# Performance work log

Hardware: AMD Instinct MI355X
Metric: run time of the kernel (lower is better)

The kernel has to match this reference:

```python
import jax, jax.numpy as jnp
import numpy as np

EMBED = 768
HEADS = 12
HEAD = EMBED // HEADS  # 64
NO_ROPE = 1
GRID = 32
S_IMG = GRID * GRID
SEQ = S_IMG + NO_ROPE
BATCH = 8
SCALE = HEAD ** -0.5


def _rope_tables():
    # VisionRotaryEmbeddingFast(dim=half_head_dim=HEAD//2, pt_seq_len=GRID)
    dim = HEAD // 2  # 32 per spatial axis
    inv_freq = 1.0 / (10000.0 ** (np.arange(0, dim, 2, dtype=np.float32) / dim))  # [dim//2]
    t = np.arange(GRID, dtype=np.float32)
    f = t[:, None] * inv_freq[None, :]              # [GRID, dim//2]
    f = np.repeat(f, 2, axis=-1)                    # interleaved pairs -> [GRID, dim]
    fh = np.broadcast_to(f[:, None, :], (GRID, GRID, dim))
    fw = np.broadcast_to(f[None, :, :], (GRID, GRID, dim))
    freqs = np.concatenate([fh, fw], axis=-1).reshape(S_IMG, HEAD)  # [S_IMG, HEAD]
    return jnp.asarray(np.cos(freqs)), jnp.asarray(np.sin(freqs))

ROPE_COS, ROPE_SIN = _rope_tables()


def _rel_pos_index():
    ch, cw = np.meshgrid(np.arange(GRID), np.arange(GRID), indexing='ij')
    coords = np.stack([ch.ravel(), cw.ravel()])          # [2, S_IMG]
    rel = coords[:, :, None] - coords[:, None, :]        # [2, S_IMG, S_IMG]
    rel = rel.transpose(1, 2, 0).astype(np.int64)
    rel[:, :, 0] += GRID - 1
    rel[:, :, 1] += GRID - 1
    rel[:, :, 0] *= 2 * GRID - 1
    return jnp.asarray(rel.sum(-1))                      # [S_IMG, S_IMG]

REL_INDEX = _rel_pos_index()


def _rotate_half(x):
    # pairs are interleaved: (d r) with r=2
    x2 = x.reshape(*x.shape[:-1], -1, 2)
    return jnp.stack([-x2[..., 1], x2[..., 0]], axis=-1).reshape(x.shape)


def _apply_rope(t):
    # t: [B, H, S, HEAD]; first NO_ROPE tokens bypass rope
    t_cls, t_img = t[:, :, :NO_ROPE, :], t[:, :, NO_ROPE:, :]
    t_img = t_img * ROPE_COS + _rotate_half(t_img) * ROPE_SIN
    return jnp.concatenate([t_cls, t_img], axis=2)


def setup_inputs() -> dict:
    key = jax.random.key(0)
    ks = jax.random.split(key, 6)
    std = EMBED ** -0.5
    return {
        'x': jax.random.normal(ks[0], (BATCH, SEQ, EMBED), jnp.float32),
        'qkv_w': jax.random.normal(ks[1], (3 * EMBED, EMBED), jnp.float32) * std,
        'qkv_b': jnp.zeros((3 * EMBED,), jnp.float32),
        'proj_w': jax.random.normal(ks[2], (EMBED, EMBED), jnp.float32) * std,
        'proj_b': jnp.zeros((EMBED,), jnp.float32),
        'rel_bias_table': jax.random.normal(ks[3], ((2 * GRID - 1) * (2 * GRID - 1), HEADS), jnp.float32) * 0.02,
        'key_padding_mask': jnp.zeros((BATCH, SEQ), jnp.bool_),
    }


def reference(x, qkv_w, qkv_b, proj_w, proj_b, rel_bias_table, key_padding_mask):
    B, S, _ = x.shape
    qkv = x @ qkv_w.T + qkv_b                                  # [B,S,3E]
    qkv = qkv.reshape(B, S, 3, HEADS, HEAD).transpose(2, 0, 3, 1, 4)
    q, k, v = qkv[0], qkv[1], qkv[2]                            # [B,H,S,D]
    q = _apply_rope(q)
    k = _apply_rope(k)
    scores = jnp.einsum('bhqd,bhkd->bhqk', q, k) * SCALE        # [B,H,S,S]
    # relative position bias on image-token sub-block
    bias = rel_bias_table[REL_INDEX]                            # [S_IMG,S_IMG,H]
    bias = bias.transpose(2, 0, 1)                              # [H,S_IMG,S_IMG]
    scores = scores.at[:, :, NO_ROPE:, NO_ROPE:].add(bias[None])
    neg = jnp.finfo(scores.dtype).min
    scores = jnp.where(key_padding_mask[:, None, None, :], neg, scores)
    attn = jax.nn.softmax(scores, axis=-1)
    ctx = jnp.einsum('bhqk,bhkd->bhqd', attn, v)
    ctx = ctx.transpose(0, 2, 1, 3).reshape(B, S, EMBED)
    return ctx @ proj_w.T + proj_b
```

## Files before the change

### kernel.cpp

```cpp
#include <hip/hip_runtime.h>
#include <math.h>

#define EMBED 768
#define NHEADS 12
#define HDIM 64
#define SEQ 1025
#define NBATCH 8
#define BHCOUNT (NBATCH*NHEADS)
#define MROWS (NBATCH*SEQ)
#define QKV_N (3*EMBED)
#define QKV_ELEMS (BHCOUNT*SEQ*HDIM)
#define BT_N 3969
#define MASKPAD 1088
#define QMUL 0.1803368801111204f
#define LOG2E 1.4426950408889634f
#define NX4 1574400
#define NW4 442368
#define NP4 147456

typedef __attribute__((ext_vector_type(8))) short bf16x8;
typedef __attribute__((ext_vector_type(4))) float f32x4;
typedef __attribute__((ext_vector_type(16))) float f32x16;
typedef __attribute__((ext_vector_type(4))) unsigned int u32x4;

#define FM3(a,b,c) fmaxf(fmaxf((a),(b)),(c))

static __device__ inline unsigned short f2bf(float f) {
    unsigned u = __float_as_uint(f);
    unsigned r = (u + 0x7FFF + ((u >> 16) & 1)) >> 16;
    return (unsigned short)r;
}

static __device__ inline unsigned int cvtpk(float a, float b) {
    unsigned int r;
    asm("v_cvt_pk_bf16_f32 %0, %1, %2" : "=v"(r) : "v"(a), "v"(b));
    return r;
}

static __device__ inline void gld16(const unsigned short* g, unsigned short* l) {
    __builtin_amdgcn_global_load_lds(
        (const __attribute__((address_space(1))) unsigned int*)g,
        (__attribute__((address_space(3))) unsigned int*)l,
        16, 0, 0);
}

__global__ __launch_bounds__(256)
void f2bf3_kernel(const float* __restrict__ x, const float* __restrict__ w,
                  const float* __restrict__ pw,
                  unsigned short* __restrict__ xbf, unsigned short* __restrict__ wbf,
                  unsigned short* __restrict__ pwbf)
{
    int i = blockIdx.x * 256 + threadIdx.x;
    const float* src; unsigned short* dst; int off;
    if (i < NX4)            { src = x;  dst = xbf;  off = i; }
    else if (i < NX4 + NW4) { src = w;  dst = wbf;  off = i - NX4; }
    else if (i < NX4 + NW4 + NP4) { src = pw; dst = pwbf; off = i - NX4 - NW4; }
    else return;
    float4 v = *reinterpret_cast<const float4*>(&src[off << 2]);
    ushort4 o;
    o.x = f2bf(v.x); o.y = f2bf(v.y); o.z = f2bf(v.z); o.w = f2bf(v.w);
    *reinterpret_cast<ushort4*>(&dst[off << 2]) = o;
}

__global__ __launch_bounds__(256)
void setup_tables_kernel(const float* __restrict__ bt, float* __restrict__ btT,
                         const unsigned char* __restrict__ m, unsigned char* __restrict__ mp,
                         float* __restrict__ cosT, float* __restrict__ sinT)
{
    const int bid = blockIdx.x, tid = threadIdx.x;
    if (bid < 256) {
        int s = (bid << 2) + (tid >> 6);
        int d = tid & 63;
        int pos = (d < 32) ? (s >> 5) : (s & 31);
        int j = (d & 31) >> 1;
        float ang = (float)pos * expf(-(float)j * 0.5756462732485115f);
        cosT[(s << 6) + d] = cosf(ang);
        sinT[(s << 6) + d] = sinf(ang);
    } else if (bid < 256 + 187) {
        int e = (bid - 256) * 256 + tid;
        if (e < NHEADS * BT_N) {
            int h = e / BT_N, idx = e - h * BT_N;
            btT[h * BT_N + idx] = bt[idx * NHEADS + h] * LOG2E;
        }
    } else {
        int b = bid - 443;
        for (int i = tid; i < MASKPAD; i += 256)
            mp[b * MASKPAD + i] = (i < SEQ) ? m[b * SEQ + i] : (unsigned char)0;
    }
}

__global__ __launch_bounds__(256)
void qkv_mfma_kernel(const unsigned short* __restrict__ xbf,
                     const unsigned short* __restrict__ wbf,
                     const float* __restrict__ bias,
                     const float* __restrict__ cosT, const float* __restrict__ sinT,
                     unsigned short* __restrict__ qout, unsigned short* __restrict__ kout,
                     unsigned short* __restrict__ vout)
{
    __shared__ unsigned short As[128][64];
    __shared__ unsigned short Bs[128][64];
    const int m0 = blockIdx.x * 128;
    const int n0 = blockIdx.y * 128;
    const int tid = threadIdx.x;
    const int w = tid >> 6, lane = tid & 63;
    const int li = lane & 15, lg = lane >> 4;
    const int wr = w >> 1, wc = w & 1;

    f32x4 acc[4][4];
    #pragma unroll
    for (int mi = 0; mi < 4; ++mi)
        #pragma unroll
        for (int nj = 0; nj < 4; ++nj) acc[mi][nj] = (f32x4){0.f, 0.f, 0.f, 0.f};

    for (int kt = 0; kt < 12; ++kt) {
        const int k0 = kt << 6;
        #pragma unroll
        for (int c = 0; c < 4; ++c) {
            const int idx = c * 256 + tid;
            const int row = idx >> 3, slot = idx & 7;
            const int ss = (slot ^ ((row ^ (row >> 3)) & 7)) << 3;
            int grow = m0 + row; if (grow > MROWS - 1) grow = MROWS - 1;
            gld16(&xbf[(long)grow * EMBED + k0 + ss], &As[0][0] + idx * 8);
            gld16(&wbf[(long)(n0 + row) * EMBED + k0 + ss], &Bs[0][0] + idx * 8);
        }
        __syncthreads();

        __builtin_amdgcn_s_setprio(1);
        #pragma unroll
        for (int kk = 0; kk < 2; ++kk) {
            bf16x8 af[4], bfr[4];
            #pragma unroll
            for (int mi = 0; mi < 4; ++mi) {
                const int row = wr * 64 + mi * 16 + li;
                const int s = ((kk * 4 + lg) ^ ((row ^ (row >> 3)) & 7)) << 3;
                af[mi] = *reinterpret_cast<const bf16x8*>(&As[row][s]);
            }
            #pragma unroll
            for (int nj = 0; nj < 4; ++nj) {
                const int row = wc * 64 + nj * 16 + li;
                const int s = ((kk * 4 + lg) ^ ((row ^ (row >> 3)) & 7)) << 3;
                bfr[nj] = *reinterpret_cast<const bf16x8*>(&Bs[row][s]);
            }
            #pragma unroll
            for (int mi = 0; mi < 4; ++mi)
                #pragma unroll
                for (int nj = 0; nj < 4; ++nj)
                    acc[mi][nj] = __builtin_amdgcn_mfma_f32_16x16x32_bf16(
                        af[mi], bfr[nj], acc[mi][nj], 0, 0, 0);
        }
        __builtin_amdgcn_s_setprio(0);
        __syncthreads();
    }

    int brow[4][4], srow[4][4];
    #pragma unroll
    for (int mi = 0; mi < 4; ++mi)
        #pragma unroll
        for (int r = 0; r < 4; ++r) {
            int m = m0 + wr * 64 + mi * 16 + lg * 4 + r;
            int mm = (m < MROWS) ? m : (MROWS - 1);
            int bb = mm / SEQ;
            brow[mi][r] = bb;
            srow[mi][r] = mm - bb * SEQ;
        }

    #pragma unroll
    for (int nj = 0; nj < 4; ++nj) {
        const int n = n0 + wc * 64 + nj * 16 + li;
        const int which = n / EMBED;
        const int nh = n - which * EMBED;
        const int h = nh >> 6, d = nh & 63;
        unsigned short* outp = (which == 0) ? qout : (which == 1) ? kout : vout;
        const float mul = (which == 0) ? QMUL : 1.0f;
        const float bn = bias[n];
        const bool dorope = which < 2;
        const float sgn = (d & 1) ? 1.f : -1.f;
        #pragma unroll
        for (int mi = 0; mi < 4; ++mi)
            #pragma unroll
            for (int r = 0; r < 4; ++r) {
                const int m = m0 + wr * 64 + mi * 16 + lg * 4 + r;
                float v = acc[mi][nj][r] + bn;
                float pv = __shfl_xor(v, 1, 64);
                if (m < MROWS) {
                    const int bb = brow[mi][r], s = srow[mi][r];
                    if (dorope && s >= 1) {
                        const int p = s - 1;
                        v = v * cosT[(p << 6) + d] + sgn * pv * sinT[(p << 6) + d];
                    }
                    outp[((long)(bb * NHEADS + h) * SEQ + s) * HDIM + d] = f2bf(v * mul);
                }
            }
    }
}

__global__ __launch_bounds__(256)
void attn_mfma_kernel(const unsigned short* __restrict__ qg,
                      const unsigned short* __restrict__ kg,
                      const unsigned short* __restrict__ vg,
                      const float* __restrict__ btT,
                      const unsigned char* __restrict__ maskpad,
                      unsigned short* __restrict__ ctx)
{
    __shared__ unsigned short Ks[2][64][64];
    __shared__ unsigned short Vts[2][64][64];

    const int i = (int)blockIdx.x;
    const int xcd = i & 7, jb = i >> 3;
    const int bh = xcd * 12 + (jb % 12);
    const int q0 = (jb / 12) * 128;
    const int b = bh / NHEADS, h = bh % NHEADS;
    const int tid = threadIdx.x;
    const int w = tid >> 6;
    const int lane = tid & 63;
    const int l31 = lane & 31;
    const int hi = lane >> 5;

    const unsigned short* qbase = qg + (long)bh * (SEQ * HDIM);
    const unsigned short* kbase = kg + (long)bh * (SEQ * HDIM);
    const unsigned short* vbase = vg + (long)bh * (SEQ * HDIM);
    const unsigned char* maskp = maskpad + b * MASKPAD;
    const float* btTh = btT + h * BT_N;

    const int sidx0 = tid, sidx1 = 256 + tid;
    const int sr0 = sidx0 >> 3, sc0 = (sidx0 & 7) << 3;
    const int sr1 = sidx1 >> 3, sc1 = (sidx1 & 7) << 3;
    const int kswz0 = ((sr0 ^ (sr0 >> 3)) & 7) << 3;
    const int kswz1 = ((sr1 ^ (sr1 >> 3)) & 7) << 3;

    gld16(&kbase[(long)sr0 * HDIM + (sc0 ^ kswz0)], &Ks[0][0][0] + sidx0 * 8);
    gld16(&kbase[(long)sr1 * HDIM + (sc1 ^ kswz1)], &Ks[0][0][0] + sidx1 * 8);
    int4 vreg[2];
    vreg[0] = *reinterpret_cast<const int4*>(&vbase[(long)sr0 * HDIM + sc0]);
    vreg[1] = *reinterpret_cast<const int4*>(&vbase[(long)sr1 * HDIM + sc1]);

    const int qrow = (w << 5) + l31;
    const int qi_l = q0 + qrow;
    const int qiq = (qi_l > SEQ - 1) ? (SEQ - 1) : qi_l;
    bf16x8 qf[4];
    #pragma unroll
    for (int s = 0; s < 4; ++s)
        qf[s] = *reinterpret_cast<const bf16x8*>(&qbase[(long)qiq * HDIM + s * 16 + hi * 8]);

    const float bq = (qi_l >= 1) ? 1.0f : 0.0f;
    int qp = qi_l - 1; if (qp < 0) qp = 0; if (qp > 1023) qp = 1023;
    const int qcode = (qp >> 5) * 63 + (qp & 31) + 1984;

    __syncthreads();
    {
        union { int4 v; unsigned short u[8]; } t0, t1;
        t0.v = vreg[0]; t1.v = vreg[1];
        const int cb30 = sc0 >> 3, cb31 = sc1 >> 3;
        #pragma unroll
        for (int e = 0; e < 8; ++e) {
            Vts[0][sc0 + e][sr0 ^ (((e ^ cb30) & 7) << 3)] = t0.u[e];
            Vts[0][sc1 + e][sr1 ^ (((e ^ cb31) & 7) << 3)] = t1.u[e];
        }
    }
    __syncthreads();

    float m_l = -1e30f, l_l = 0.f;
    f32x16 acco[2];
    #pragma unroll
    for (int r = 0; r < 16; ++r) { acco[0][r] = 0.f; acco[1][r] = 0.f; }

    int kcb[2][4];
    for (int kt = 0; kt < 17; ++kt) {
        const int k0 = kt * 64;
        const int cur = kt & 1;

        if (kt < 16) {
            const int k0n = k0 + 64;
            vreg[0] = (k0n + sr0 < SEQ)
                ? *reinterpret_cast<const int4*>(&vbase[(long)(k0n + sr0) * HDIM + sc0])
                : make_int4(0, 0, 0, 0);
            vreg[1] = (k0n + sr1 < SEQ)
                ? *reinterpret_cast<const int4*>(&vbase[(long)(k0n + sr1) * HDIM + sc1])
                : make_int4(0, 0, 0, 0);
            int ki0 = k0n + sr0; if (ki0 > SEQ - 1) ki0 = SEQ - 1;
            int ki1 = k0n + sr1; if (ki1 > SEQ - 1) ki1 = SEQ - 1;
            gld16(&kbase[(long)ki0 * HDIM + (sc0 ^ kswz0)], &Ks[cur ^ 1][0][0] + sidx0 * 8);
            gld16(&kbase[(long)ki1 * HDIM + (sc1 ^ kswz1)], &Ks[cur ^ 1][0][0] + sidx1 * 8);
        }

        float bvf[2][16];
        unsigned int b4[2][4];
        unsigned int anym = 0;
        const bool interior = (kt >= 1 && kt <= 15);
        if (interior) {
            const uint4 ma_ = *reinterpret_cast<const uint4*>(&maskp[k0]);
            const uint4 mb_ = *reinterpret_cast<const uint4*>(&maskp[k0 + 16]);
            const uint4 mc_ = *reinterpret_cast<const uint4*>(&maskp[k0 + 32]);
            const uint4 md_ = *reinterpret_cast<const uint4*>(&maskp[k0 + 48]);
            anym = (ma_.x | ma_.y | ma_.z | ma_.w) | (mb_.x | mb_.y | mb_.z | mb_.w) |
                   (mc_.x | mc_.y | mc_.z | mc_.w) | (md_.x | md_.y | md_.z | md_.w);
            #pragma unroll
            for (int j = 0; j < 2; ++j)
                #pragma unroll
                for (int t = 0; t < 4; ++t) {
                    kcb[j][t] += 126;
                    const int base = qcode - kcb[j][t];
                    if (t == 0 && hi == 0) {
                        float4 f = *reinterpret_cast<const float4*>(&btTh[base - 34]);
                        bvf[j][0] = btTh[base]; bvf[j][1] = f.z;
                        bvf[j][2] = f.y;        bvf[j][3] = f.x;
                    } else {
                        float4 f = *reinterpret_cast<const float4*>(&btTh[base - 3]);
                        bvf[j][t * 4 + 0] = f.w; bvf[j][t * 4 + 1] = f.z;
                        bvf[j][t * 4 + 2] = f.y; bvf[j][t * 4 + 3] = f.x;
                    }
                }
        } else {
            #pragma unroll
            for (int j = 0; j < 2; ++j)
                #pragma unroll
                for (int t = 0; t < 4; ++t) {
                    unsigned int bb = 0;
                    #pragma unroll
                    for (int ri = 0; ri < 4; ++ri) {
                        const int ki = k0 + j * 32 + t * 8 + hi * 4 + ri;
                        const int kic = (ki > SEQ - 1) ? (SEQ - 1) : ki;
                        unsigned int dead = (ki >= SEQ) ? 1u : (unsigned int)maskp[kic];
                        bb |= (dead ? 1u : 0u) << (ri * 8);
                        int kp = ki - 1; if (kp < 0) kp = 0; if (kp > 1023) kp = 1023;
                        const int kcv = (kp >> 5) * 63 + (kp & 31);
                        bvf[j][t * 4 + ri] = btTh[qcode - kcv];
                    }
                    b4[j][t] = bb;
                    if (kt == 0) {
                        const int kp0 = j * 32 + t * 8 + hi * 4 - 1;
                        kcb[j][t] = (kp0 >> 5) * 63 + (kp0 & 31);
                    }
                }
        }

        if (kt == 0 && hi == 0) bvf[0][0] = 0.0f;
        f32x16 accs[2];
        #pragma unroll
        for (int j = 0; j < 2; ++j)
            #pragma unroll
            for (int r = 0; r < 16; ++r)
                accs[j][r] = bvf[j][r] * bq;
        __builtin_amdgcn_s_setprio(1);
        #pragma unroll
        for (int j = 0; j < 2; ++j) {
            const int rswz = ((l31 ^ (j * 4 + (l31 >> 3))) & 7) << 3;
            const unsigned short* krow = &Ks[cur][j * 32 + l31][0];
            #pragma unroll
            for (int s = 0; s < 4; ++s) {
                bf16x8 kf = *reinterpret_cast<const bf16x8*>(&krow[(s * 16 + hi * 8) ^ rswz]);
                accs[j] = __builtin_amdgcn_mfma_f32_32x32x16_bf16(kf, qf[s], accs[j], 0, 0, 0);
            }
        }
        __builtin_amdgcn_s_setprio(0);

        if (interior) {
            if (anym) {
                #pragma unroll
                for (int j = 0; j < 2; ++j)
                    #pragma unroll
                    for (int t = 0; t < 4; ++t)
                        #pragma unroll
                        for (int ri = 0; ri < 4; ++ri)
                            if (maskp[k0 + j * 32 + t * 8 + hi * 4 + ri])
                                accs[j][t * 4 + ri] = -1e30f;
            }
        } else {
            if (__any((b4[0][0] | b4[0][1] | b4[0][2] | b4[0][3] |
                       b4[1][0] | b4[1][1] | b4[1][2] | b4[1][3]) != 0)) {
                #pragma unroll
                for (int j = 0; j < 2; ++j)
                    #pragma unroll
                    for (int r = 0; r < 16; ++r)
                        if ((b4[j][r >> 2] >> ((r & 3) * 8)) & 0xFF) accs[j][r] = -1e30f;
            }
        }

        float t0 = FM3(accs[0][0],  accs[0][1],  accs[0][2]);
        float t1 = FM3(accs[0][3],  accs[0][4],  accs[0][5]);
        float t2 = FM3(accs[0][6],  accs[0][7],  accs[0][8]);
        float t3 = FM3(accs[0][9],  accs[0][10], accs[0][11]);
        float t4 = FM3(accs[0][12], accs[0][13], accs[0][14]);
        float t5 = FM3(accs[0][15], accs[1][0],  accs[1][1]);
        float t6 = FM3(accs[1][2],  accs[1][3],  accs[1][4]);
        float t7 = FM3(accs[1][5],  accs[1][6],  accs[1][7]);
        float t8 = FM3(accs[1][8],  accs[1][9],  accs[1][10]);
        float t9 = FM3(accs[1][11], accs[1][12], accs[1][13]);
        float u0 = FM3(t0, t1, t2);
        float u1 = FM3(t3, t4, t5);
        float u2 = FM3(t6, t7, t8);
        float u3 = FM3(t9, accs[1][14], accs[1][15]);
        float mx = fmaxf(FM3(u0, u1, u2), u3);
        mx = fmaxf(mx, __shfl_xor(mx, 32, 64));
        if (__any(mx > m_l + 8.0f)) {
            const float mnew = fmaxf(m_l, mx);
            const float alpha = __builtin_amdgcn_exp2f(m_l - mnew);
            #pragma unroll
            for (int r = 0; r < 16; ++r) {
                const float al = __shfl(alpha, (r & 3) + 8 * (r >> 2) + 4 * hi, 64);
                acco[0][r] *= al;
                acco[1][r] *= al;
            }
            l_l *= alpha;
            m_l = mnew;
        }
        float rs = 0.f;
        #pragma unroll
        for (int j = 0; j < 2; ++j)
            #pragma unroll
            for (int r = 0; r < 16; ++r) {
                accs[j][r] = __builtin_amdgcn_exp2f(accs[j][r] - m_l);
                rs += accs[j][r];
            }
        rs += __shfl_xor(rs, 32, 64);
        l_l += rs;

        unsigned int W[2][8];
        #pragma unroll
        for (int j = 0; j < 2; ++j)
            #pragma unroll
            for (int p = 0; p < 8; ++p)
                W[j][p] = cvtpk(accs[j][2 * p], accs[j][2 * p + 1]);
        #pragma unroll
        for (int j = 0; j < 2; ++j)
            #pragma unroll
            for (int sg = 0; sg < 2; ++sg) {
                unsigned int a0 = W[j][4 * sg + 0], a2 = W[j][4 * sg + 2];
                asm volatile("v_permlane32_swap_b32 %0, %1" : "+v"(a0), "+v"(a2));
                W[j][4 * sg + 0] = a0; W[j][4 * sg + 2] = a2;
                unsigned int a1 = W[j][4 * sg + 1], a3 = W[j][4 * sg + 3];
                asm volatile("v_permlane32_swap_b32 %0, %1" : "+v"(a1), "+v"(a3));
                W[j][4 * sg + 1] = a1; W[j][4 * sg + 3] = a3;
            }

        __builtin_amdgcn_s_setprio(1);
        #pragma unroll
        for (int j2 = 0; j2 < 2; ++j2) {
            const int vswz = ((l31 ^ (j2 * 4 + (l31 >> 3))) & 7) << 3;
            const unsigned short* vrow = &Vts[cur][j2 * 32 + l31][0];
            #pragma unroll
            for (int s = 0; s < 4; ++s) {
                bf16x8 vf = *reinterpret_cast<const bf16x8*>(&vrow[(s * 16 + hi * 8) ^ vswz]);
                u32x4 aw;
                aw[0] = W[s >> 1][4 * (s & 1) + 0];
                aw[1] = W[s >> 1][4 * (s & 1) + 1];
                aw[2] = W[s >> 1][4 * (s & 1) + 2];
                aw[3] = W[s >> 1][4 * (s & 1) + 3];
                bf16x8 pa = __builtin_bit_cast(bf16x8, aw);
                acco[j2] = __builtin_amdgcn_mfma_f32_32x32x16_bf16(pa, vf, acco[j2], 0, 0, 0);
            }
        }
        __builtin_amdgcn_s_setprio(0);

        if (kt < 16) {
            union { int4 v; unsigned short u[8]; } t0v, t1v;
            t0v.v = vreg[0]; t1v.v = vreg[1];
            const int cb30 = sc0 >> 3, cb31 = sc1 >> 3;
            #pragma unroll
            for (int e = 0; e < 8; ++e) {
                Vts[cur ^ 1][sc0 + e][sr0 ^ (((e ^ cb30) & 7) << 3)] = t0v.u[e];
                Vts[cur ^ 1][sc1 + e][sr1 ^ (((e ^ cb31) & 7) << 3)] = t1v.u[e];
            }
            __syncthreads();
        }
    }

    #pragma unroll
    for (int r = 0; r < 16; ++r) {
        const int ql = (r & 3) + 8 * (r >> 2) + 4 * hi;
        const float lb = __shfl(l_l, ql, 64);
        const int qi = q0 + (w << 5) + ql;
        if (qi < SEQ) {
            const float inv = 1.0f / lb;
            ctx[(long)(b * SEQ + qi) * EMBED + h * HDIM + l31] = f2bf(acco[0][r] * inv);
            ctx[(long)(b * SEQ + qi) * EMBED + h * HDIM + 32 + l31] = f2bf(acco[1][r] * inv);
        }
    }
}

__global__ __launch_bounds__(256)
void proj_mfma_kernel(const unsigned short* __restrict__ ctxbf,
                      const unsigned short* __restrict__ pwbf,
                      const float* __restrict__ bias, float* __restrict__ out)
{
    __shared__ unsigned short As[128][64];
    __shared__ unsigned short Bs[128][64];
    const int m0 = blockIdx.x * 128;
    const int n0 = blockIdx.y * 128;
    const int tid = threadIdx.x;
    const int w = tid >> 6, lane = tid & 63;
    const int li = lane & 15, lg = lane >> 4;
    const int wr = w >> 1, wc = w & 1;

    f32x4 acc[4][4];
    #pragma unroll
    for (int mi = 0; mi < 4; ++mi)
        #pragma unroll
        for (int nj = 0; nj < 4; ++nj) acc[mi][nj] = (f32x4){0.f, 0.f, 0.f, 0.f};

    for (int kt = 0; kt < 12; ++kt) {
        const int k0 = kt << 6;
        #pragma unroll
        for (int c = 0; c < 4; ++c) {
            const int idx = c * 256 + tid;
            const int row = idx >> 3, slot = idx & 7;
            const int ss = (slot ^ ((row ^ (row >> 3)) & 7)) << 3;
            int grow = m0 + row; if (grow > MROWS - 1) grow = MROWS - 1;
            gld16(&ctxbf[(long)grow * EMBED + k0 + ss], &As[0][0] + idx * 8);
            gld16(&pwbf[(long)(n0 + row) * EMBED + k0 + ss], &Bs[0][0] + idx * 8);
        }
        __syncthreads();

        __builtin_amdgcn_s_setprio(1);
        #pragma unroll
        for (int kk = 0; kk < 2; ++kk) {
            bf16x8 af[4], bfr[4];
            #pragma unroll
            for (int mi = 0; mi < 4; ++mi) {
                const int row = wr * 64 + mi * 16 + li;
                const int s = ((kk * 4 + lg) ^ ((row ^ (row >> 3)) & 7)) << 3;
                af[mi] = *reinterpret_cast<const bf16x8*>(&As[row][s]);
            }
            #pragma unroll
            for (int nj = 0; nj < 4; ++nj) {
                const int row = wc * 64 + nj * 16 + li;
                const int s = ((kk * 4 + lg) ^ ((row ^ (row >> 3)) & 7)) << 3;
                bfr[nj] = *reinterpret_cast<const bf16x8*>(&Bs[row][s]);
            }
            #pragma unroll
            for (int mi = 0; mi < 4; ++mi)
                #pragma unroll
                for (int nj = 0; nj < 4; ++nj)
                    acc[mi][nj] = __builtin_amdgcn_mfma_f32_16x16x32_bf16(
                        af[mi], bfr[nj], acc[mi][nj], 0, 0, 0);
        }
        __builtin_amdgcn_s_setprio(0);
        __syncthreads();
    }

    #pragma unroll
    for (int nj = 0; nj < 4; ++nj) {
        const int n = n0 + wc * 64 + nj * 16 + li;
        const float bn = bias[n];
        #pragma unroll
        for (int mi = 0; mi < 4; ++mi)
            #pragma unroll
            for (int r = 0; r < 4; ++r) {
                const int m = m0 + wr * 64 + mi * 16 + lg * 4 + r;
                if (m < MROWS)
                    out[(long)m * EMBED + n] = acc[mi][nj][r] + bn;
            }
    }
}

extern "C" void kernel_launch(void* const* d_in, const int* in_sizes, int n_in,
                              void* d_out, int out_size, void* d_ws, size_t ws_size,
                              hipStream_t stream) {
    const float* x       = (const float*)d_in[0];
    const float* qkv_w   = (const float*)d_in[1];
    const float* qkv_b   = (const float*)d_in[2];
    const float* proj_w  = (const float*)d_in[3];
    const float* proj_b  = (const float*)d_in[4];
    const float* rel_bt  = (const float*)d_in[5];
    const unsigned char* kmask = (const unsigned char*)d_in[6];
    float* out = (float*)d_out;

    unsigned short* qbuf  = (unsigned short*)d_ws;
    unsigned short* kbuf  = qbuf + QKV_ELEMS;
    unsigned short* vbuf  = kbuf + QKV_ELEMS;
    unsigned short* ctxbf = vbuf + QKV_ELEMS;
    unsigned short* xbf   = ctxbf + QKV_ELEMS;
    unsigned short* wbf   = xbf + QKV_ELEMS;
    unsigned short* pwbf  = wbf + QKV_N * EMBED;
    float* cosT = (float*)(pwbf + EMBED * EMBED);
    float* sinT = cosT + 1024 * HDIM;
    float* btT  = sinT + 1024 * HDIM;
    unsigned char* maskpad = (unsigned char*)(btT + NHEADS * BT_N);

    const int ntot4 = NX4 + NW4 + NP4;
    f2bf3_kernel<<<(ntot4 + 255) / 256, 256, 0, stream>>>(x, qkv_w, proj_w, xbf, wbf, pwbf);
    setup_tables_kernel<<<256 + 187 + NBATCH, 256, 0, stream>>>(
        rel_bt, btT, kmask, maskpad, cosT, sinT);

    qkv_mfma_kernel<<<dim3((MROWS + 127) / 128, QKV_N / 128), 256, 0, stream>>>(
        xbf, wbf, qkv_b, cosT, sinT, qbuf, kbuf, vbuf);
    attn_mfma_kernel<<<9 * BHCOUNT, 256, 0, stream>>>(
        qbuf, kbuf, vbuf, btT, maskpad, ctxbf);
    proj_mfma_kernel<<<dim3((MROWS + 127) / 128, EMBED / 128), 256, 0, stream>>>(
        ctxbf, pwbf, proj_b, out);
}
```

Baseline: 216.4 us.

## Software-pipeline PV matmul of previous tile under current QK matmul

The P·V MFMA for key tile kt-1 now runs right after the Q·K MFMA of tile kt, so the two matrix phases can overlap with the softmax work in between. This removes the serial wait of softmax followed by PV inside each iteration. V tiles move to a triple-buffered shared-memory ring so the previous tile stays readable while the next one is written, and an epilogue finishes the last PV. The costs are an extra 8 KB of LDS and the packed probabilities kept live across iterations, which raises register pressure and may lower occupancy.

```diff
diff --git a/kernel.cpp b/kernel.cpp
--- a/kernel.cpp
+++ b/kernel.cpp
@@ -203,7 +203,7 @@
                       unsigned short* __restrict__ ctx)
 {
     __shared__ unsigned short Ks[2][64][64];
-    __shared__ unsigned short Vts[2][64][64];
+    __shared__ unsigned short Vts[3][64][64];
 
     const int i = (int)blockIdx.x;
     const int xcd = i & 7, jb = i >> 3;
@@ -264,10 +264,13 @@
     #pragma unroll
     for (int r = 0; r < 16; ++r) { acco[0][r] = 0.f; acco[1][r] = 0.f; }
 
+    unsigned int Wp[2][8];
     int kcb[2][4];
     for (int kt = 0; kt < 17; ++kt) {
         const int k0 = kt * 64;
         const int cur = kt & 1;
+        const int vdrain = (kt + 1) % 3;
+        const int vprev  = (kt + 2) % 3;
 
         if (kt < 16) {
             const int k0n = k0 + 64;
@@ -352,6 +355,24 @@
                 accs[j] = __builtin_amdgcn_mfma_f32_32x32x16_bf16(kf, qf[s], accs[j], 0, 0, 0);
             }
         }
+        if (kt >= 1) {
+            #pragma unroll
+            for (int j2 = 0; j2 < 2; ++j2) {
+                const int vswz = ((l31 ^ (j2 * 4 + (l31 >> 3))) & 7) << 3;
+                const unsigned short* vrow = &Vts[vprev][j2 * 32 + l31][0];
+                #pragma unroll
+                for (int s = 0; s < 4; ++s) {
+                    bf16x8 vf = *reinterpret_cast<const bf16x8*>(&vrow[(s * 16 + hi * 8) ^ vswz]);
+                    u32x4 aw;
+                    aw[0] = Wp[s >> 1][4 * (s & 1) + 0];
+                    aw[1] = Wp[s >> 1][4 * (s & 1) + 1];
+                    aw[2] = Wp[s >> 1][4 * (s & 1) + 2];
+                    aw[3] = Wp[s >> 1][4 * (s & 1) + 3];
+                    bf16x8 pa = __builtin_bit_cast(bf16x8, aw);
+                    acco[j2] = __builtin_amdgcn_mfma_f32_32x32x16_bf16(pa, vf, acco[j2], 0, 0, 0);
+                }
+            }
+        }
         __builtin_amdgcn_s_setprio(0);
 
         if (interior) {
@@ -415,42 +436,22 @@
         rs += __shfl_xor(rs, 32, 64);
         l_l += rs;
 
-        unsigned int W[2][8];
         #pragma unroll
         for (int j = 0; j < 2; ++j)
             #pragma unroll
             for (int p = 0; p < 8; ++p)
-                W[j][p] = cvtpk(accs[j][2 * p], accs[j][2 * p + 1]);
+                Wp[j][p] = cvtpk(accs[j][2 * p], accs[j][2 * p + 1]);
         #pragma unroll
         for (int j = 0; j < 2; ++j)
             #pragma unroll
             for (int sg = 0; sg < 2; ++sg) {
-                unsigned int a0 = W[j][4 * sg + 0], a2 = W[j][4 * sg + 2];
+                unsigned int a0 = Wp[j][4 * sg + 0], a2 = Wp[j][4 * sg + 2];
                 asm volatile("v_permlane32_swap_b32 %0, %1" : "+v"(a0), "+v"(a2));
-                W[j][4 * sg + 0] = a0; W[j][4 * sg + 2] = a2;
-                unsigned int a1 = W[j][4 * sg + 1], a3 = W[j][4 * sg + 3];
+                Wp[j][4 * sg + 0] = a0; Wp[j][4 * sg + 2] = a2;
+                unsigned int a1 = Wp[j][4 * sg + 1], a3 = Wp[j][4 * sg + 3];
                 asm volatile("v_permlane32_swap_b32 %0, %1" : "+v"(a1), "+v"(a3));
-                W[j][4 * sg + 1] = a1; W[j][4 * sg + 3] = a3;
-            }
-
-        __builtin_amdgcn_s_setprio(1);
-        #pragma unroll
-        for (int j2 = 0; j2 < 2; ++j2) {
-            const int vswz = ((l31 ^ (j2 * 4 + (l31 >> 3))) & 7) << 3;
-            const unsigned short* vrow = &Vts[cur][j2 * 32 + l31][0];
-            #pragma unroll
-            for (int s = 0; s < 4; ++s) {
-                bf16x8 vf = *reinterpret_cast<const bf16x8*>(&vrow[(s * 16 + hi * 8) ^ vswz]);
-                u32x4 aw;
-                aw[0] = W[s >> 1][4 * (s & 1) + 0];
-                aw[1] = W[s >> 1][4 * (s & 1) + 1];
-                aw[2] = W[s >> 1][4 * (s & 1) + 2];
-                aw[3] = W[s >> 1][4 * (s & 1) + 3];
-                bf16x8 pa = __builtin_bit_cast(bf16x8, aw);
-                acco[j2] = __builtin_amdgcn_mfma_f32_32x32x16_bf16(pa, vf, acco[j2], 0, 0, 0);
-            }
-        }
-        __builtin_amdgcn_s_setprio(0);
+                Wp[j][4 * sg + 1] = a1; Wp[j][4 * sg + 3] = a3;
+            }
 
         if (kt < 16) {
             union { int4 v; unsigned short u[8]; } t0v, t1v;
@@ -458,10 +459,29 @@
             const int cb30 = sc0 >> 3, cb31 = sc1 >> 3;
             #pragma unroll
             for (int e = 0; e < 8; ++e) {
-                Vts[cur ^ 1][sc0 + e][sr0 ^ (((e ^ cb30) & 7) << 3)] = t0v.u[e];
-                Vts[cur ^ 1][sc1 + e][sr1 ^ (((e ^ cb31) & 7) << 3)] = t1v.u[e];
+                Vts[vdrain][sc0 + e][sr0 ^ (((e ^ cb30) & 7) << 3)] = t0v.u[e];
+                Vts[vdrain][sc1 + e][sr1 ^ (((e ^ cb31) & 7) << 3)] = t1v.u[e];
             }
             __syncthreads();
+        }
+    }
+
+    {
+        #pragma unroll
+        for (int j2 = 0; j2 < 2; ++j2) {
+            const int vswz = ((l31 ^ (j2 * 4 + (l31 >> 3))) & 7) << 3;
+            const unsigned short* vrow = &Vts[1][j2 * 32 + l31][0];
+            #pragma unroll
+            for (int s = 0; s < 4; ++s) {
+                bf16x8 vf = *reinterpret_cast<const bf16x8*>(&vrow[(s * 16 + hi * 8) ^ vswz]);
+                u32x4 aw;
+                aw[0] = Wp[s >> 1][4 * (s & 1) + 0];
+                aw[1] = Wp[s >> 1][4 * (s & 1) + 1];
+                aw[2] = Wp[s >> 1][4 * (s & 1) + 2];
+                aw[3] = Wp[s >> 1][4 * (s & 1) + 3];
+                bf16x8 pa = __builtin_bit_cast(bf16x8, aw);
+                acco[j2] = __builtin_amdgcn_mfma_f32_32x32x16_bf16(pa, vf, acco[j2], 0, 0, 0);
+            }
         }
     }
 
```

Result: slower. 296.3 us (+36.9%).
